# Optimization experiments

Hardware: AMD Instinct MI355X
Metric: run time of the kernel (lower is better)

Reference implementation:

```python
import jax, jax.numpy as jnp
import numpy as np

MULT = 0.001      # DEFAULT_MULTIPLIER
N_ITERS = 9       # self.N
N_K = 4           # self.l
BINARY = ('mul', 'add')  # original binary_ops_list order


def _valid_pairs(nc, r, lc):
    # replicate flag logic over (i, j) candidate pairs
    nri = N_ITERS - r
    out = []
    for i in range(nc - 1):
        for j in range(i + 1, nc):
            if nri == lc - 1:
                flag = i >= 3
            elif nri == lc:
                flag = j >= 3
            else:
                flag = nri > lc
            if flag:
                out.append((i, j))
    return out


def _act(name, res):
    if name == 'sigmoid':
        return MULT * jax.nn.sigmoid(res)
    if name == 'tanh':
        return MULT * jnp.tanh(res)
    if name == 'minus':
        return 1.0 - res
    return res  # identity


def run_cell(x, h_prev, L, R, b, w, plan=None):
    """Faithful RRNNforGRUCell tree-structure search.
    record mode (plan=None): data-dependent decisions taken concretely (eager).
    replay mode (plan given): purely differentiable jnp replay of recorded plan.
    """
    record = plan is None
    if record:
        plan = []
    xv = x.reshape(-1)
    hv = h_prev.reshape(-1)
    H = xv.shape[0]
    zero = jnp.zeros((H,), dtype=xv.dtype)
    G = []            # max_vector per iteration
    second = []       # second-ranked vector per iteration
    comp_src = []     # G-indices backing current components_list
    for r in range(N_ITERS):
        cand = [xv, hv, zero] + [G[g] for g in comp_src]
        nc = len(cand)
        C = jnp.stack(cand)                       # (nc, H)
        CL = jnp.einsum('ch,khd->ckd', C, L)      # (nc, 4, H) all s_i @ L_k
        CR = jnp.einsum('ch,khd->ckd', C, R)      # (nc, 4, H) all s_j @ R_k
        V = []
        if record:
            entries = []
            for (i, j) in _valid_pairs(nc, r, len(comp_src)):
                for k in range(N_K):
                    for bf in BINARY:
                        if bf == 'mul':
                            res = CL[i, k] * CR[j, k] + b[k]
                        else:
                            res = CL[i, k] + CR[j, k] + b[k]
                        if float(jnp.max(jnp.abs(res))) >= 1.0:
                            acts = ('sigmoid', 'tanh')
                        else:
                            acts = ('sigmoid', 'tanh', 'minus', 'identity')
                        for a in acts:
                            V.append(_act(a, res))
                            entries.append((i, j, k, bf, a))
        else:
            entries = plan[r]['entries']
            cache = {}
            for (i, j, k, bf, a) in entries:
                key = (i, j, k, bf)
                if key not in cache:
                    if bf == 'mul':
                        cache[key] = CL[i, k] * CR[j, k] + b[k]
                    else:
                        cache[key] = CL[i, k] + CR[j, k] + b[k]
                V.append(_act(a, cache[key]))
        Vs = jnp.stack(V)          # (nV, H)
        scores = Vs @ w            # (nV,) scoring Linear(H,1,bias=False)
        if record:
            s = np.asarray(scores)
            max_idx = int(np.argmax(s))
            # position of the element ranked second-smallest (original code)
            second_idx = int(np.where(np.argsort(s) == 1)[0][0])
            plan.append({'entries': entries, 'max_idx': max_idx, 'second_idx': second_idx})
        else:
            max_idx = plan[r]['max_idx']
            second_idx = plan[r]['second_idx']
        probs = jax.nn.softmax(scores)
        # NOTE: replicates original bug: loop uses stale `i` == nc-2, so every
        # v is weighted by probabilities[nc-2].
        max_vec = probs[nc - 2] * Vs.sum(axis=0)
        second.append(V[second_idx])
        G.append(max_vec)
        i, j = entries[max_idx][0], entries[max_idx][1]
        if i > 2 and j > 2:
            comp_src[i - 3] = r
            del comp_src[j - 3]
        elif i <= 2 and j > 2:
            comp_src[j - 3] = r
        else:
            comp_src.append(r)
    Gs = jnp.stack(G)                       # (9, H)
    out = (Gs[-1], Gs, Gs @ w, jnp.stack(second) @ w)
    return (out, plan) if record else out


def setup_inputs() -> dict:
    key = jax.random.key(0)
    ks = jax.random.split(key, 6)
    H = 2048
    return {
        'x': jax.random.normal(ks[0], (1, H), jnp.float32),
        'h_prev': jax.random.normal(ks[1], (1, H), jnp.float32),
        'L': MULT * jax.random.normal(ks[2], (N_K, H, H), jnp.float32),
        'R': MULT * jax.random.normal(ks[3], (N_K, H, H), jnp.float32),
        'b': MULT * jax.random.normal(ks[4], (N_K, H), jnp.float32),
        'w': jax.random.normal(ks[5], (H,), jnp.float32),
    }


def reference(x, h_prev, L, R, b, w):
    # returns (h_next, G_stack [9,H], scores of G [9], second_scores [9])
    out, _ = run_cell(x, h_prev, L, R, b, w)
    return out
```

## Files before the change

kernel.cpp:

```cpp
#include <hip/hip_runtime.h>
#include <math.h>

#define HDIM 2048
#define NK 4
#define NIT 9
#define NSID 11
#define MAXPAIRS 36
#define MAXBASES (MAXPAIRS*8)

#define CACHE_SZ (NSID*2*NK*HDIM)
#define OFF_CACHE 0
#define OFF_AMAX   (OFF_CACHE + CACHE_SZ)
#define OFF_DOTR_D (OFF_AMAX + MAXBASES)
#define OFF_DOTS_D (OFF_DOTR_D + 2*MAXBASES)
#define OFF_DOTT_D (OFF_DOTS_D + 2*MAXBASES)
#define PLAN_SZ 152
#define OFF_PLAN0 (OFF_DOTT_D + 2*MAXBASES)
#define OFF_PLAN1 (OFF_PLAN0 + PLAN_SZ)
#define OFF_STATE (OFF_PLAN1 + PLAN_SZ)
#define OFF_SUMW_D (OFF_STATE + 16)
#define OFF_GT8   (OFF_SUMW_D + 16)
#define OFF_PART  (OFF_GT8 + 8*HDIM)

__device__ __forceinline__ float wredmax(float v){
#pragma unroll
  for(int o=32;o;o>>=1) v = fmaxf(v,__shfl_down(v,o,64));
  return v;
}
__device__ __forceinline__ float wredsum(float v){
#pragma unroll
  for(int o=32;o;o>>=1) v += __shfl_down(v,o,64);
  return v;
}
__device__ __forceinline__ double wredsumd(double v){
#pragma unroll
  for(int o=32;o;o>>=1) v += __shfl_down(v,o,64);
  return v;
}

__device__ void build_plan(int r, int lc, const int* cs, int* plan){
  int nc = 3 + lc;
  int nri = NIT - r;
  int np = 0;
  for(int i=0;i<nc-1;i++){
    for(int j=i+1;j<nc;j++){
      bool flag;
      if (nri == lc-1)      flag = (i>=3);
      else if (nri == lc)   flag = (j>=3);
      else                  flag = (nri > lc);
      if(flag){
        plan[8+np]            = i;
        plan[8+MAXPAIRS+np]   = j;
        plan[8+2*MAXPAIRS+np] = (i<3)? i : 3+cs[i-3];
        plan[8+3*MAXPAIRS+np] = (j<3)? j : 3+cs[j-3];
        np++;
      }
    }
  }
  plan[0]=nc; plan[1]=np; plan[2]=np*8;
}

__global__ __launch_bounds__(512) void kvecmat(const float* __restrict__ va,
                                               const float* __restrict__ vb,
                                               const float* __restrict__ w,
                                               const float* __restrict__ L,
                                               const float* __restrict__ R,
                                               float* __restrict__ ws,
                                               int nvec){
  int bid = blockIdx.x;
  int tid = threadIdx.x;
  int nmain = nvec << 8;
  if (bid >= nmain){
    int ib = bid - nmain;
    for(int i = ib*512+tid; i < 8*HDIM; i += 32*512)
      ws[OFF_CACHE + 16*HDIM + i] = 0.f;
    if (ib == 0){
      double s = 0.0;
      for(int d=tid; d<HDIM; d+=512) s += (double)w[d];
      s = wredsumd(s);
      __shared__ double red[8];
      int wv = tid>>6, ln = tid&63;
      if(!ln) red[wv]=s;
      __syncthreads();
      if(tid==0){
        double t2=0.0;
        for(int q=0;q<8;q++) t2 += red[q];
        *(double*)(ws + OFF_SUMW_D) = t2;
        int* st = (int*)(ws + OFF_STATE);
        for(int q=0;q<=8;q++) st[q]=0;
        build_plan(0, 0, st+1, (int*)(ws + OFF_PLAN0));
      }
    }
    return;
  }
  int vec   = bid >> 8;
  int b     = bid & 255;
  int combo = b >> 5;
  int hc    = b & 31;
  const float* v = vec ? vb : va;
  __shared__ float vs[64];
  if (tid < 64) vs[tid] = v[hc*64 + tid];
  __syncthreads();
  int m = combo>>2, k = combo&3;
  const float* M = (m==0?L:R) + (size_t)k*HDIM*HDIM + (size_t)hc*64*HDIM + tid*4;
  float ax=0.f, ay=0.f, az=0.f, aw=0.f;
#pragma unroll 16
  for(int h=0; h<64; h++){
    const float4 f = *reinterpret_cast<const float4*>(M + (size_t)h*HDIM);
    float vv = vs[h];
    ax = fmaf(vv, f.x, ax); ay = fmaf(vv, f.y, ay);
    az = fmaf(vv, f.z, az); aw = fmaf(vv, f.w, aw);
  }
  float4 o; o.x=ax; o.y=ay; o.z=az; o.w=aw;
  *reinterpret_cast<float4*>(ws + OFF_PART + ((size_t)(vec*8+combo)*32 + hc)*HDIM + tid*4) = o;
}

__global__ __launch_bounds__(256) void kreduce(float* __restrict__ ws, int sid0){
  int b = blockIdx.x;
  int vec = b>>6, rem = b&63;
  int combo = rem>>3, dc8 = rem&7;
  int d = dc8*256 + threadIdx.x;
  const float* p = ws + OFF_PART + (size_t)(vec*8+combo)*32*HDIM + d;
  float s = 0.f;
#pragma unroll
  for(int hc=0; hc<32; hc++) s += p[(size_t)hc*HDIM];
  int m = combo>>2, k = combo&3;
  int sid = sid0 + vec;
  ws[OFF_CACHE + ((size_t)(sid*2+m)*NK + k)*HDIM + d] = s;
}

__global__ __launch_bounds__(256) void kbaseaccum(const float* __restrict__ bvec,
                                                  const float* __restrict__ w,
                                                  float* __restrict__ ws, int par){
  const int* plan = (const int*)(ws + (par ? OFF_PLAN1 : OFF_PLAN0));
  int nb = plan[2];
  if (blockIdx.x < MAXBASES){
    int t = blockIdx.x;
    if (t >= nb) return;
    int p = t>>3, k=(t>>1)&3, bf=t&1;
    int si = plan[8+2*MAXPAIRS+p], sj = plan[8+3*MAXPAIRS+p];
    const float* CL = ws + OFF_CACHE + ((size_t)(si*2+0)*NK + k)*HDIM;
    const float* CR = ws + OFF_CACHE + ((size_t)(sj*2+1)*NK + k)*HDIM;
    const float* bk = bvec + (size_t)k*HDIM;
    float am=0.f; double dr=0.0, ds=0.0, dt=0.0;
    for(int d=threadIdx.x; d<HDIM; d+=256){
      float a = CL[d], c = CR[d];
      float res = (bf==0) ? __fadd_rn(__fmul_rn(a,c), bk[d])
                          : __fadd_rn(__fadd_rn(a,c), bk[d]);
      float wd = w[d];
      am = fmaxf(am, fabsf(res));
      float sg = 1.0f/(1.0f+expf(-res));
      float th = tanhf(res);
      dr += (double)res*(double)wd;
      ds += (double)sg *(double)wd;
      dt += (double)th *(double)wd;
    }
    am = wredmax(am); dr = wredsumd(dr); ds = wredsumd(ds); dt = wredsumd(dt);
    __shared__ double redd[4][3];
    __shared__ float  redm[4];
    int wv = threadIdx.x>>6, ln = threadIdx.x&63;
    if(!ln){ redm[wv]=am; redd[wv][0]=dr; redd[wv][1]=ds; redd[wv][2]=dt; }
    __syncthreads();
    if(!threadIdx.x){
      float A=redm[0]; double Dr=redd[0][0], Ds=redd[0][1], Dt=redd[0][2];
      for(int q=1;q<4;q++){ A=fmaxf(A,redm[q]); Dr+=redd[q][0]; Ds+=redd[q][1]; Dt+=redd[q][2]; }
      ws[OFF_AMAX+t]=A;
      ((double*)(ws+OFF_DOTR_D))[t]=Dr;
      ((double*)(ws+OFF_DOTS_D))[t]=Ds;
      ((double*)(ws+OFF_DOTT_D))[t]=Dt;
    }
  } else {
    int bid2 = blockIdx.x - MAXBASES;
    int bc = bid2 >> 3;
    int db = bid2 & 7;
    int d = db*256 + threadIdx.x;
    float acc = 0.f;
    for(int t=bc; t<nb; t+=8){
      int p=t>>3, k=(t>>1)&3, bf=t&1;
      int si = plan[8+2*MAXPAIRS+p], sj = plan[8+3*MAXPAIRS+p];
      float a = ws[OFF_CACHE + ((size_t)(si*2+0)*NK+k)*HDIM + d];
      float c = ws[OFF_CACHE + ((size_t)(sj*2+1)*NK+k)*HDIM + d];
      float res = (bf==0) ? (a*c + bvec[(size_t)k*HDIM+d]) : (a + c + bvec[(size_t)k*HDIM+d]);
      float ex  = __expf(-res);
      float sig = 1.0f/(1.0f+ex);
      float ex2 = ex*ex;
      float th  = (1.0f-ex2)/(1.0f+ex2);
      acc += sig + th;
    }
    ws[OFF_GT8 + (size_t)bc*HDIM + d] = acc;
  }
}

__global__ __launch_bounds__(256) void kselfin(const float* __restrict__ w,
                                               float* __restrict__ ws,
                                               float* __restrict__ out, int r){
  __shared__ double s4[MAXBASES][4];
  __shared__ int    sna[MAXBASES];
  __shared__ double tval[256];
  __shared__ int    tidx[256];
  __shared__ double tz[256];
  __shared__ int    tcnt[256];
  __shared__ double sh_smax;
  __shared__ float  sh_psel;
  __shared__ int    sh_c4;
  int par = r & 1;
  int* plan = (int*)(ws + (par ? OFF_PLAN1 : OFF_PLAN0));
  int nc = plan[0];
  int nb = plan[2];
  double sumw = *(const double*)(ws + OFF_SUMW_D);
  const double* DR = (const double*)(ws+OFF_DOTR_D);
  const double* DS = (const double*)(ws+OFF_DOTS_D);
  const double* DT = (const double*)(ws+OFF_DOTT_D);
  int tid = threadIdx.x;
  for(int t=tid; t<nb; t+=256){
    float A  = ws[OFF_AMAX+t];
    double Dr = DR[t], Ds = DS[t], Dt = DT[t];
    sna[t] = (A < 1.0f) ? 4 : 2;
    s4[t][0] = 0.001*Ds;
    s4[t][1] = 0.001*Dt;
    s4[t][2] = sumw - Dr;
    s4[t][3] = Dr;
  }
  __syncthreads();
  double best = -1e300; int bidx = 1<<30;
  for(int q=tid; q<nb*4; q+=256){
    int t=q>>2, a=q&3;
    if (a < sna[t]){
      double v = s4[t][a];
      if (v > best || (v==best && q < bidx)){ best=v; bidx=q; }
    }
  }
  tval[tid]=best; tidx[tid]=bidx;
  __syncthreads();
  if (tid==0){
    double bb=tval[0]; int bi=tidx[0];
    for(int u=1;u<256;u++)
      if (tval[u] > bb || (tval[u]==bb && tidx[u] < bi)){ bb=tval[u]; bi=tidx[u]; }
    sh_smax = bb;
    tidx[0] = bi;
  }
  __syncthreads();
  double smax = sh_smax;
  double s1 = s4[0][1];
  double z = 0.0; int cnt = 0;
  for(int q=tid; q<nb*4; q+=256){
    int t=q>>2, a=q&3;
    if (a < sna[t]){
      double v = s4[t][a];
      z += exp(v - smax);
      cnt += (v < s1) ? 1 : 0;
    }
  }
  tz[tid]=z; tcnt[tid]=cnt;
  __syncthreads();
  if (tid==0){
    int bi = tidx[0];
    double Z=0.0; int rank=0;
    for(int u=0;u<256;u++){ Z += tz[u]; rank += tcnt[u]; }
    int need = nc-2, e=0; double s_sel=0.0;
    for(int t=0;t<nb;t++){
      int n = sna[t];
      if (need < e+n){ s_sel = s4[t][need-e]; break; }
      e += n;
    }
    double psel = exp(s_sel - smax) / Z;
    int e2=0; double ssec=0.0;
    for(int t=0;t<nb;t++){
      int n = sna[t];
      if (rank < e2+n){ ssec = s4[t][rank-e2]; break; }
      e2 += n;
    }
    out[10*HDIM + 9 + r] = (float)ssec;
    int c4=0;
    for(int t=0;t<nb;t++) c4 += (sna[t]==4) ? 1 : 0;
    int mt = bi>>2;
    int mp = mt>>3;
    int ci = plan[8+mp], cj = plan[8+MAXPAIRS+mp];
    sh_psel = (float)psel;
    sh_c4   = c4;
    int* st = (int*)(ws + OFF_STATE);
    int lc = st[0];
    int* cs = st+1;
    if (ci>2 && cj>2){
      cs[ci-3] = r;
      for(int q2=cj-3; q2<lc-1; q2++) cs[q2]=cs[q2+1];
      lc--;
    } else if (ci<=2 && cj>2){
      cs[cj-3] = r;
    } else {
      cs[lc] = r; lc++;
    }
    st[0]=lc;
    if (r+1 < NIT)
      build_plan(r+1, lc, cs, (int*)(ws + ((par^1) ? OFF_PLAN1 : OFF_PLAN0)));
  }
  __syncthreads();
  float psel = sh_psel;
  float c4f  = (float)sh_c4;
  float dot = 0.f;
#pragma unroll
  for(int q=0;q<8;q++){
    int d = q*256 + tid;
    float s = 0.f;
#pragma unroll
    for(int bc=0; bc<8; bc++) s += ws[OFF_GT8 + (size_t)bc*HDIM + d];
    float g = psel * (0.001f*s + c4f);
    out[HDIM + (size_t)r*HDIM + d] = g;
    if (r == NIT-1) out[d] = g;
    dot = fmaf(g, w[d], dot);
  }
  dot = wredsum(dot);
  __shared__ float redf[4];
  int wv = tid>>6, ln = tid&63;
  if(!ln) redf[wv]=dot;
  __syncthreads();
  if(!tid) out[10*HDIM + r] = redf[0]+redf[1]+redf[2]+redf[3];
}

extern "C" void kernel_launch(void* const* d_in, const int* in_sizes, int n_in,
                              void* d_out, int out_size, void* d_ws, size_t ws_size,
                              hipStream_t stream){
  const float* x = (const float*)d_in[0];
  const float* h = (const float*)d_in[1];
  const float* L = (const float*)d_in[2];
  const float* R = (const float*)d_in[3];
  const float* b = (const float*)d_in[4];
  const float* w = (const float*)d_in[5];
  float* out = (float*)d_out;
  float* ws  = (float*)d_ws;

  kvecmat<<<512+32,512,0,stream>>>(x, h, w, L, R, ws, 2);
  kreduce<<<128,256,0,stream>>>(ws, 0);
  for(int r=0;r<NIT;r++){
    if (r > 0){
      kvecmat<<<256,512,0,stream>>>(out + HDIM + (size_t)(r-1)*HDIM, nullptr, w, L, R, ws, 1);
      kreduce<<<64,256,0,stream>>>(ws, 3+(r-1));
    }
    kbaseaccum<<<MAXBASES+64,256,0,stream>>>(b, w, ws, r&1);
    kselfin<<<1,256,0,stream>>>(w, ws, out, r);
  }
}
```

Before: 562.2 us.

## Fuse reduce and select stages into producers via last-block atomic tickets

Merges the separate partial-sum reduction kernel into the matvec kernel and the single-block selection kernel into the base-accumulation kernel. In each case the last block to finish, found with an atomic ticket counter and thread fences, does the follow-up work. This cuts the kernel launches per iteration from four to two. Initialization moves into its own small kernel, and the matvec inner loop is software-pipelined with double-buffered float4 loads and sched barriers. The cost is atomic traffic and a serial tail in the last block, plus counter-reset correctness that depends on the fences.

```diff
diff --git a/kernel.cpp b/kernel.cpp
--- a/kernel.cpp
+++ b/kernel.cpp
@@ -7,6 +7,8 @@
 #define NSID 11
 #define MAXPAIRS 36
 #define MAXBASES (MAXPAIRS*8)
+#define NACC 64
+#define NBS (MAXBASES + NACC)
 
 #define CACHE_SZ (NSID*2*NK*HDIM)
 #define OFF_CACHE 0
@@ -19,7 +21,8 @@
 #define OFF_PLAN1 (OFF_PLAN0 + PLAN_SZ)
 #define OFF_STATE (OFF_PLAN1 + PLAN_SZ)
 #define OFF_SUMW_D (OFF_STATE + 16)
-#define OFF_GT8   (OFF_SUMW_D + 16)
+#define OFF_CNT   (OFF_SUMW_D + 2)
+#define OFF_GT8   (OFF_CNT + 18)
 #define OFF_PART  (OFF_GT8 + 8*HDIM)
 
 __device__ __forceinline__ float wredmax(float v){
@@ -60,120 +63,158 @@
   plan[0]=nc; plan[1]=np; plan[2]=np*8;
 }
 
+__global__ __launch_bounds__(256) void kinit(const float* __restrict__ w,
+                                             float* __restrict__ ws){
+  int tid = threadIdx.x;
+  for(int i=blockIdx.x*256+tid; i<8*HDIM; i+=8*256)
+    ws[OFF_CACHE + 16*HDIM + i] = 0.f;
+  if (blockIdx.x == 7 && tid < 17)
+    ((int*)(ws + OFF_CNT))[tid] = 0;
+  if (blockIdx.x == 0){
+    double s = 0.0;
+    for(int d=tid; d<HDIM; d+=256) s += (double)w[d];
+    s = wredsumd(s);
+    __shared__ double red[4];
+    int wv = tid>>6, ln = tid&63;
+    if(!ln) red[wv]=s;
+    __syncthreads();
+    if(tid==0){
+      *(double*)(ws + OFF_SUMW_D) = red[0]+red[1]+red[2]+red[3];
+      int* st = (int*)(ws + OFF_STATE);
+      for(int q=0;q<=8;q++) st[q]=0;
+      build_plan(0, 0, st+1, (int*)(ws + OFF_PLAN0));
+    }
+  }
+}
+
+#define LOAD8(DST, G) do { \
+  _Pragma("unroll") \
+  for(int j=0;j<8;j++) DST[j] = *reinterpret_cast<const float4*>(M + (size_t)((G)*8+j)*HDIM); \
+} while(0)
+#define FMA8(SRC, G) do { \
+  _Pragma("unroll") \
+  for(int j=0;j<8;j++){ float vv = vs[(G)*8+j]; \
+    ax = fmaf(vv, SRC[j].x, ax); ay = fmaf(vv, SRC[j].y, ay); \
+    az = fmaf(vv, SRC[j].z, az); aw = fmaf(vv, SRC[j].w, aw); } \
+} while(0)
+#define SB() __builtin_amdgcn_sched_barrier(0)
+
 __global__ __launch_bounds__(512) void kvecmat(const float* __restrict__ va,
                                                const float* __restrict__ vb,
-                                               const float* __restrict__ w,
                                                const float* __restrict__ L,
                                                const float* __restrict__ R,
                                                float* __restrict__ ws,
-                                               int nvec){
+                                               int sid0){
   int bid = blockIdx.x;
   int tid = threadIdx.x;
-  int nmain = nvec << 8;
-  if (bid >= nmain){
-    int ib = bid - nmain;
-    for(int i = ib*512+tid; i < 8*HDIM; i += 32*512)
-      ws[OFF_CACHE + 16*HDIM + i] = 0.f;
-    if (ib == 0){
-      double s = 0.0;
-      for(int d=tid; d<HDIM; d+=512) s += (double)w[d];
-      s = wredsumd(s);
-      __shared__ double red[8];
-      int wv = tid>>6, ln = tid&63;
-      if(!ln) red[wv]=s;
-      __syncthreads();
-      if(tid==0){
-        double t2=0.0;
-        for(int q=0;q<8;q++) t2 += red[q];
-        *(double*)(ws + OFF_SUMW_D) = t2;
-        int* st = (int*)(ws + OFF_STATE);
-        for(int q=0;q<=8;q++) st[q]=0;
-        build_plan(0, 0, st+1, (int*)(ws + OFF_PLAN0));
-      }
-    }
-    return;
-  }
   int vec   = bid >> 8;
   int b     = bid & 255;
   int combo = b >> 5;
   int hc    = b & 31;
   const float* v = vec ? vb : va;
   __shared__ float vs[64];
+  __shared__ int tkt;
   if (tid < 64) vs[tid] = v[hc*64 + tid];
   __syncthreads();
   int m = combo>>2, k = combo&3;
   const float* M = (m==0?L:R) + (size_t)k*HDIM*HDIM + (size_t)hc*64*HDIM + tid*4;
   float ax=0.f, ay=0.f, az=0.f, aw=0.f;
-#pragma unroll 16
-  for(int h=0; h<64; h++){
-    const float4 f = *reinterpret_cast<const float4*>(M + (size_t)h*HDIM);
-    float vv = vs[h];
-    ax = fmaf(vv, f.x, ax); ay = fmaf(vv, f.y, ay);
-    az = fmaf(vv, f.z, az); aw = fmaf(vv, f.w, aw);
-  }
+  float4 A[8], B[8];
+  LOAD8(A,0);
+  LOAD8(B,1); SB();
+  FMA8(A,0);
+  LOAD8(A,2); SB();
+  FMA8(B,1);
+  LOAD8(B,3); SB();
+  FMA8(A,2);
+  LOAD8(A,4); SB();
+  FMA8(B,3);
+  LOAD8(B,5); SB();
+  FMA8(A,4);
+  LOAD8(A,6); SB();
+  FMA8(B,5);
+  LOAD8(B,7); SB();
+  FMA8(A,6);
+  FMA8(B,7);
   float4 o; o.x=ax; o.y=ay; o.z=az; o.w=aw;
   *reinterpret_cast<float4*>(ws + OFF_PART + ((size_t)(vec*8+combo)*32 + hc)*HDIM + tid*4) = o;
-}
-
-__global__ __launch_bounds__(256) void kreduce(float* __restrict__ ws, int sid0){
-  int b = blockIdx.x;
-  int vec = b>>6, rem = b&63;
-  int combo = rem>>3, dc8 = rem&7;
-  int d = dc8*256 + threadIdx.x;
-  const float* p = ws + OFF_PART + (size_t)(vec*8+combo)*32*HDIM + d;
-  float s = 0.f;
-#pragma unroll
-  for(int hc=0; hc<32; hc++) s += p[(size_t)hc*HDIM];
-  int m = combo>>2, k = combo&3;
-  int sid = sid0 + vec;
-  ws[OFF_CACHE + ((size_t)(sid*2+m)*NK + k)*HDIM + d] = s;
-}
-
-__global__ __launch_bounds__(256) void kbaseaccum(const float* __restrict__ bvec,
-                                                  const float* __restrict__ w,
-                                                  float* __restrict__ ws, int par){
-  const int* plan = (const int*)(ws + (par ? OFF_PLAN1 : OFF_PLAN0));
+  __threadfence();
+  if (tid == 0) tkt = atomicAdd((int*)(ws + OFF_CNT) + (vec*8+combo), 1);
+  __syncthreads();
+  if (tkt != 31) return;
+  __threadfence();
+  if (tid == 0) ((int*)(ws + OFF_CNT))[vec*8+combo] = 0;
+  const float* P = ws + OFF_PART + (size_t)(vec*8+combo)*32*HDIM + tid*4;
+  float sx=0.f, sy=0.f, sz=0.f, sw=0.f;
+#pragma unroll
+  for(int q=0; q<32; q++){
+    const float4 pf = *reinterpret_cast<const float4*>(P + (size_t)q*HDIM);
+    sx += pf.x; sy += pf.y; sz += pf.z; sw += pf.w;
+  }
+  float4 so; so.x=sx; so.y=sy; so.z=sz; so.w=sw;
+  *reinterpret_cast<float4*>(ws + OFF_CACHE + ((size_t)((sid0+vec)*2+m)*NK + k)*HDIM + tid*4) = so;
+}
+
+__global__ __launch_bounds__(256) void kbasesel(const float* __restrict__ bvec,
+                                                const float* __restrict__ w,
+                                                float* __restrict__ ws,
+                                                float* __restrict__ out, int r){
+  __shared__ double s4[MAXBASES][4];
+  __shared__ int    sna[MAXBASES];
+  __shared__ double tval[256];
+  __shared__ int    tidx[256];
+  __shared__ double tz[256];
+  __shared__ int    tcnt[256];
+  __shared__ double sh_smax;
+  __shared__ float  sh_psel;
+  __shared__ int    sh_c4;
+  __shared__ int    tkt;
+  int par = r & 1;
+  int* plan = (int*)(ws + (par ? OFF_PLAN1 : OFF_PLAN0));
+  int nc = plan[0];
   int nb = plan[2];
+  int tid = threadIdx.x;
   if (blockIdx.x < MAXBASES){
     int t = blockIdx.x;
-    if (t >= nb) return;
-    int p = t>>3, k=(t>>1)&3, bf=t&1;
-    int si = plan[8+2*MAXPAIRS+p], sj = plan[8+3*MAXPAIRS+p];
-    const float* CL = ws + OFF_CACHE + ((size_t)(si*2+0)*NK + k)*HDIM;
-    const float* CR = ws + OFF_CACHE + ((size_t)(sj*2+1)*NK + k)*HDIM;
-    const float* bk = bvec + (size_t)k*HDIM;
-    float am=0.f; double dr=0.0, ds=0.0, dt=0.0;
-    for(int d=threadIdx.x; d<HDIM; d+=256){
-      float a = CL[d], c = CR[d];
-      float res = (bf==0) ? __fadd_rn(__fmul_rn(a,c), bk[d])
-                          : __fadd_rn(__fadd_rn(a,c), bk[d]);
-      float wd = w[d];
-      am = fmaxf(am, fabsf(res));
-      float sg = 1.0f/(1.0f+expf(-res));
-      float th = tanhf(res);
-      dr += (double)res*(double)wd;
-      ds += (double)sg *(double)wd;
-      dt += (double)th *(double)wd;
-    }
-    am = wredmax(am); dr = wredsumd(dr); ds = wredsumd(ds); dt = wredsumd(dt);
-    __shared__ double redd[4][3];
-    __shared__ float  redm[4];
-    int wv = threadIdx.x>>6, ln = threadIdx.x&63;
-    if(!ln){ redm[wv]=am; redd[wv][0]=dr; redd[wv][1]=ds; redd[wv][2]=dt; }
-    __syncthreads();
-    if(!threadIdx.x){
-      float A=redm[0]; double Dr=redd[0][0], Ds=redd[0][1], Dt=redd[0][2];
-      for(int q=1;q<4;q++){ A=fmaxf(A,redm[q]); Dr+=redd[q][0]; Ds+=redd[q][1]; Dt+=redd[q][2]; }
-      ws[OFF_AMAX+t]=A;
-      ((double*)(ws+OFF_DOTR_D))[t]=Dr;
-      ((double*)(ws+OFF_DOTS_D))[t]=Ds;
-      ((double*)(ws+OFF_DOTT_D))[t]=Dt;
+    if (t < nb){
+      int p = t>>3, k=(t>>1)&3, bf=t&1;
+      int si = plan[8+2*MAXPAIRS+p], sj = plan[8+3*MAXPAIRS+p];
+      const float* CL = ws + OFF_CACHE + ((size_t)(si*2+0)*NK + k)*HDIM;
+      const float* CR = ws + OFF_CACHE + ((size_t)(sj*2+1)*NK + k)*HDIM;
+      const float* bk = bvec + (size_t)k*HDIM;
+      float am=0.f; double dr=0.0, ds=0.0, dt=0.0;
+      for(int d=tid; d<HDIM; d+=256){
+        float a = CL[d], c = CR[d];
+        float res = (bf==0) ? __fadd_rn(__fmul_rn(a,c), bk[d])
+                            : __fadd_rn(__fadd_rn(a,c), bk[d]);
+        float wd = w[d];
+        am = fmaxf(am, fabsf(res));
+        float sg = 1.0f/(1.0f+expf(-res));
+        float th = tanhf(res);
+        dr += (double)res*(double)wd;
+        ds += (double)sg *(double)wd;
+        dt += (double)th *(double)wd;
+      }
+      am = wredmax(am); dr = wredsumd(dr); ds = wredsumd(ds); dt = wredsumd(dt);
+      __shared__ double redd[4][3];
+      __shared__ float  redm[4];
+      int wv = tid>>6, ln = tid&63;
+      if(!ln){ redm[wv]=am; redd[wv][0]=dr; redd[wv][1]=ds; redd[wv][2]=dt; }
+      __syncthreads();
+      if(!tid){
+        float A=redm[0]; double Dr=redd[0][0], Ds=redd[0][1], Dt=redd[0][2];
+        for(int q=1;q<4;q++){ A=fmaxf(A,redm[q]); Dr+=redd[q][0]; Ds+=redd[q][1]; Dt+=redd[q][2]; }
+        ws[OFF_AMAX+t]=A;
+        ((double*)(ws+OFF_DOTR_D))[t]=Dr;
+        ((double*)(ws+OFF_DOTS_D))[t]=Ds;
+        ((double*)(ws+OFF_DOTT_D))[t]=Dt;
+      }
     }
   } else {
     int bid2 = blockIdx.x - MAXBASES;
     int bc = bid2 >> 3;
     int db = bid2 & 7;
-    int d = db*256 + threadIdx.x;
+    int d = db*256 + tid;
     float acc = 0.f;
     for(int t=bc; t<nb; t+=8){
       int p=t>>3, k=(t>>1)&3, bf=t&1;
@@ -189,29 +230,16 @@
     }
     ws[OFF_GT8 + (size_t)bc*HDIM + d] = acc;
   }
-}
-
-__global__ __launch_bounds__(256) void kselfin(const float* __restrict__ w,
-                                               float* __restrict__ ws,
-                                               float* __restrict__ out, int r){
-  __shared__ double s4[MAXBASES][4];
-  __shared__ int    sna[MAXBASES];
-  __shared__ double tval[256];
-  __shared__ int    tidx[256];
-  __shared__ double tz[256];
-  __shared__ int    tcnt[256];
-  __shared__ double sh_smax;
-  __shared__ float  sh_psel;
-  __shared__ int    sh_c4;
-  int par = r & 1;
-  int* plan = (int*)(ws + (par ? OFF_PLAN1 : OFF_PLAN0));
-  int nc = plan[0];
-  int nb = plan[2];
+  __threadfence();
+  if (tid == 0) tkt = atomicAdd((int*)(ws + OFF_CNT) + 16, 1);
+  __syncthreads();
+  if (tkt != NBS-1) return;
+  __threadfence();
+  if (tid == 0) ((int*)(ws + OFF_CNT))[16] = 0;
   double sumw = *(const double*)(ws + OFF_SUMW_D);
   const double* DR = (const double*)(ws+OFF_DOTR_D);
   const double* DS = (const double*)(ws+OFF_DOTS_D);
   const double* DT = (const double*)(ws+OFF_DOTT_D);
-  int tid = threadIdx.x;
   for(int t=tid; t<nb; t+=256){
     float A  = ws[OFF_AMAX+t];
     double Dr = DR[t], Ds = DS[t], Dt = DT[t];
@@ -329,14 +357,11 @@
   float* out = (float*)d_out;
   float* ws  = (float*)d_ws;
 
-  kvecmat<<<512+32,512,0,stream>>>(x, h, w, L, R, ws, 2);
-  kreduce<<<128,256,0,stream>>>(ws, 0);
+  kinit<<<8,256,0,stream>>>(w, ws);
+  kvecmat<<<512,512,0,stream>>>(x, h, L, R, ws, 0);
   for(int r=0;r<NIT;r++){
-    if (r > 0){
-      kvecmat<<<256,512,0,stream>>>(out + HDIM + (size_t)(r-1)*HDIM, nullptr, w, L, R, ws, 1);
-      kreduce<<<64,256,0,stream>>>(ws, 3+(r-1));
-    }
-    kbaseaccum<<<MAXBASES+64,256,0,stream>>>(b, w, ws, r&1);
-    kselfin<<<1,256,0,stream>>>(w, ws, out, r);
-  }
-}
+    if (r > 0)
+      kvecmat<<<256,512,0,stream>>>(out + HDIM + (size_t)(r-1)*HDIM, nullptr, L, R, ws, 3+(r-1));
+    kbasesel<<<NBS,256,0,stream>>>(b, w, ws, out, r);
+  }
+}
```

Result: slower. 1.357 ms (+141.4%).
